# Kernel tuning notes

Measured on AMD Instinct MI355X. Metric: run time of the kernel, lower is better.

Reference implementation:

```python
import jax, jax.numpy as jnp
import numpy as np

NUM_HEADS = 12


def setup_inputs() -> dict:
    key = jax.random.key(0)
    ks = jax.random.split(key, 6)
    C = 768
    hd = C // NUM_HEADS  # 64
    H = W = 32
    x = jax.random.normal(ks[0], (4, H, W, C), dtype=jnp.float32)
    # Linear weights stored as (in, out) so y = x @ W (+ b)
    Wqkv = jax.random.normal(ks[1], (C, 3 * C), dtype=jnp.float32) * 0.02
    Wproj = jax.random.normal(ks[2], (C, C), dtype=jnp.float32) * 0.02
    bproj = jax.random.normal(ks[3], (C,), dtype=jnp.float32) * 0.02
    rel_pos_h = jax.random.normal(ks[4], (2 * H - 1, hd), dtype=jnp.float32) * 0.02
    rel_pos_w = jax.random.normal(ks[5], (2 * W - 1, hd), dtype=jnp.float32) * 0.02
    return {"x": x, "Wqkv": Wqkv, "Wproj": Wproj, "bproj": bproj,
            "rel_pos_h": rel_pos_h, "rel_pos_w": rel_pos_w}


def _get_rel_pos(size: int, rel_pos: jnp.ndarray) -> jnp.ndarray:
    # q_size == k_size == size; table already has 2*size-1 entries -> no interpolation
    coords = jnp.arange(size)[:, None] - jnp.arange(size)[None, :] + (size - 1)
    return rel_pos[coords]  # (size, size, head_dim)


def reference(x, Wqkv, Wproj, bproj, rel_pos_h, rel_pos_w):
    B, H, W, C = x.shape
    hn = NUM_HEADS
    hd = C // hn
    scale = hd ** (-0.5)
    S = H * W

    qkv = x @ Wqkv                                   # (B,H,W,3C)
    qkv = qkv.reshape(B, S, 3, hn, hd)
    qkv = jnp.transpose(qkv, (2, 0, 3, 1, 4)).reshape(3, B * hn, S, hd)
    q, k, v = qkv[0], qkv[1], qkv[2]                 # each (B*hn, S, hd)

    # decomposed relative position bias
    Rh = _get_rel_pos(H, rel_pos_h)                  # (H,H,hd)
    Rw = _get_rel_pos(W, rel_pos_w)                  # (W,W,hd)
    r_q = q.reshape(B * hn, H, W, hd)
    rel_h = jnp.einsum('bhwc,hkc->bhwk', r_q, Rh)    # (B*hn,H,W,H)
    rel_w = jnp.einsum('bhwc,wkc->bhwk', r_q, Rw)    # (B*hn,H,W,W)
    bias = rel_h[..., :, None] + rel_w[..., None, :] # (B*hn,H,W,H,W)
    bias = bias.reshape(B * hn, S, S)

    scores = scale * jnp.einsum('bqc,bkc->bqk', q, k) + bias
    attn = jax.nn.softmax(scores, axis=-1)
    out = jnp.einsum('bqk,bkc->bqc', attn, v)        # (B*hn,S,hd)

    out = out.reshape(B, hn, H, W, hd)
    out = jnp.transpose(out, (0, 2, 3, 1, 4)).reshape(B, H, W, C)
    return out @ Wproj + bproj
```

## Files before the change

kernel.cpp:

```cpp
#include <hip/hip_runtime.h>
#include <stddef.h>

typedef __bf16 bf16x8 __attribute__((ext_vector_type(8)));
typedef __bf16 bf16x4 __attribute__((ext_vector_type(4)));
typedef _Float16 f16x4 __attribute__((ext_vector_type(4)));
typedef float  f32x4  __attribute__((ext_vector_type(4)));

#define MFMA16(a, b, c) __builtin_amdgcn_mfma_f32_16x16x32_bf16((a), (b), (c), 0, 0, 0)
#define MFMA16H(a, b, c) __builtin_amdgcn_mfma_f32_16x16x16f16((a), (b), (c), 0, 0, 0)

__device__ __forceinline__ void gload_lds16(const void* gsrc, void* ldst) {
    __builtin_amdgcn_global_load_lds(
        (__attribute__((address_space(1))) void*)gsrc,
        (__attribute__((address_space(3))) void*)ldst,
        16, 0, 0);
}

__global__ void prep_kernel(const float* __restrict__ x, __bf16* __restrict__ xbf,
                            const float* __restrict__ Wqkv, __bf16* __restrict__ WqkvT,
                            const float* __restrict__ Wproj, __bf16* __restrict__ WprojT) {
    __shared__ float tile[32][33];
    const int bx = blockIdx.x, tid = threadIdx.x;
    if (bx < 3072) {
        int i = bx * 256 + tid;
        float4 v = ((const float4*)x)[i];
        bf16x4 o = {(__bf16)v.x, (__bf16)v.y, (__bf16)v.z, (__bf16)v.w};
        ((bf16x4*)xbf)[i] = o;
        return;
    }
    const float* in; __bf16* out; int R, C, c0, r0;
    if (bx < 4800) { int bb = bx - 3072; in = Wqkv;  out = WqkvT;  R = 768; C = 2304;
                     c0 = (bb % 72) * 32; r0 = (bb / 72) * 32; }
    else           { int bb = bx - 4800; in = Wproj; out = WprojT; R = 768; C = 768;
                     c0 = (bb % 24) * 32; r0 = (bb / 24) * 32; }
    const int tx = tid & 31, ty = tid >> 5;
#pragma unroll
    for (int i = 0; i < 32; i += 8)
        tile[ty + i][tx] = in[(size_t)(r0 + ty + i) * C + c0 + tx];
    __syncthreads();
#pragma unroll
    for (int i = 0; i < 32; i += 8)
        out[(size_t)(c0 + ty + i) * R + r0 + tx] = (__bf16)tile[tx][ty + i];
}

template<int BM, int BN>
__device__ __forceinline__ void gemm_core_bk64(
    const __bf16* __restrict__ A, const __bf16* __restrict__ Bt, int K,
    int m0, int n0, __bf16* aT, __bf16* bT, f32x4 (&acc)[BM/32][BN/32]) {
    const int tid  = threadIdx.x;
    const int wid  = tid >> 6, lane = tid & 63;
    const int quad = lane >> 4, l16 = lane & 15;
    const int wm = (wid >> 1) * (BM / 2), wn = (wid & 1) * (BN / 2);
    const int r_in = lane >> 3;
    const int cswz = ((lane & 7) ^ r_in) * 8;
    const __bf16* gA = A  + (size_t)(m0 + wid * 8 + r_in) * K + cswz;
    const __bf16* gB = Bt + (size_t)(n0 + wid * 8 + r_in) * K + cswz;
    const int sA = (l16 & 7);
    for (int k0 = 0; k0 < K; k0 += 64) {
        __syncthreads();
#pragma unroll
        for (int j = 0; j < BM / 32; j++)
            gload_lds16(gA + (size_t)(j * 32) * K + k0, aT + (j * 32 + wid * 8) * 64);
#pragma unroll
        for (int j = 0; j < BN / 32; j++)
            gload_lds16(gB + (size_t)(j * 32) * K + k0, bT + (j * 32 + wid * 8) * 64);
        __syncthreads();
#pragma unroll
        for (int kh = 0; kh < 2; kh++) {
            bf16x8 af[BM / 32], bfr[BN / 32];
            const int slot = ((kh * 4 + quad) ^ sA) << 3;
#pragma unroll
            for (int t = 0; t < BM / 32; t++)
                af[t]  = *(const bf16x8*)(aT + (wm + t * 16 + l16) * 64 + slot);
#pragma unroll
            for (int t = 0; t < BN / 32; t++)
                bfr[t] = *(const bf16x8*)(bT + (wn + t * 16 + l16) * 64 + slot);
#pragma unroll
            for (int rt = 0; rt < BM / 32; rt++)
#pragma unroll
                for (int ct = 0; ct < BN / 32; ct++)
                    acc[rt][ct] = MFMA16(af[rt], bfr[ct], acc[rt][ct]);
        }
    }
}

__global__ __launch_bounds__(256, 3)
void gemm_qkv_kernel(const __bf16* __restrict__ A, const __bf16* __restrict__ Bt,
                     __bf16* __restrict__ qb, __bf16* __restrict__ kb,
                     _Float16* __restrict__ vtb) {
    __shared__ __bf16 aT[8192], bT[6144];
    f32x4 acc[4][3];
#pragma unroll
    for (int i = 0; i < 4; i++)
#pragma unroll
        for (int j = 0; j < 3; j++) { f32x4 z = {0.f, 0.f, 0.f, 0.f}; acc[i][j] = z; }
    const int m0 = blockIdx.x * 128, n0 = blockIdx.y * 96;
    gemm_core_bk64<128, 96>(A, Bt, 768, m0, n0, aT, bT, acc);
    const int tid = threadIdx.x, wid = tid >> 6, lane = tid & 63;
    const int quad = lane >> 4, l16 = lane & 15;
    const int wm = (wid >> 1) * 64, wn = (wid & 1) * 48;
    const float KSCALE = 0.18033688f;
#pragma unroll
    for (int rt = 0; rt < 4; rt++)
#pragma unroll
        for (int ct = 0; ct < 3; ct++) {
            const int ng = n0 + wn + ct * 16 + l16;
            const int which = ng / 768;
            const int rem = ng - which * 768;
            const int hh = rem >> 6, d = rem & 63;
#pragma unroll
            for (int r = 0; r < 4; r++) {
                const int mg = m0 + wm + rt * 16 + quad * 4 + r;
                const int b = mg >> 10, s = mg & 1023;
                const int bh = b * 12 + hh;
                if (which == 0)      qb[((size_t)bh * 1024 + s) * 64 + d] = (__bf16)acc[rt][ct][r];
                else if (which == 1) kb[((size_t)bh * 1024 + s) * 64 + d] = (__bf16)(acc[rt][ct][r] * KSCALE);
                else                 vtb[((size_t)bh * 64 + d) * 1024 + s] = (_Float16)acc[rt][ct][r];
            }
        }
}

__global__ __launch_bounds__(256, 3)
void gemm_proj_kernel(const __bf16* __restrict__ A, const __bf16* __restrict__ Bt,
                      const float* __restrict__ bias, float* __restrict__ out) {
    __shared__ __bf16 aT[4096], bT[6144];
    f32x4 acc[2][3];
#pragma unroll
    for (int i = 0; i < 2; i++)
#pragma unroll
        for (int j = 0; j < 3; j++) { f32x4 z = {0.f, 0.f, 0.f, 0.f}; acc[i][j] = z; }
    const int m0 = blockIdx.x * 64, n0 = blockIdx.y * 96;
    gemm_core_bk64<64, 96>(A, Bt, 768, m0, n0, aT, bT, acc);
    const int tid = threadIdx.x, wid = tid >> 6, lane = tid & 63;
    const int quad = lane >> 4, l16 = lane & 15;
    const int wm = (wid >> 1) * 32, wn = (wid & 1) * 48;
#pragma unroll
    for (int rt = 0; rt < 2; rt++)
#pragma unroll
        for (int ct = 0; ct < 3; ct++) {
            const int ng = n0 + wn + ct * 16 + l16;
            const float bb = bias[ng];
#pragma unroll
            for (int r = 0; r < 4; r++) {
                const int mg = m0 + wm + rt * 16 + quad * 4 + r;
                out[(size_t)mg * 768 + ng] = acc[rt][ct][r] + bb;
            }
        }
}

__global__ __launch_bounds__(256, 3)
void attn_kernel(const __bf16* __restrict__ q, const __bf16* __restrict__ kk,
                 const _Float16* __restrict__ vt, const float* __restrict__ rph,
                 const float* __restrict__ rpw, __bf16* __restrict__ aout) {
    __shared__ __bf16   kbuf2[2][4096];
    __shared__ _Float16 vbuf2[2][4096];
    __shared__ float    relh[64][33];
    const int tid = threadIdx.x, wid = tid >> 6, lane = tid & 63;
    const int quad = lane >> 4, l16 = lane & 15;
    const int bh = blockIdx.x, qt = blockIdx.y;
    const int b = bh / 12, hh = bh - b * 12;
    const int q0 = qt * 64;
    const int w0 = wid * 16;
    const int h = qt * 2 + (wid >> 1);
    const float LOG2E = 1.44269504f;

    const __bf16* qp = q + ((size_t)bh * 1024 + q0 + w0 + l16) * 64;
    bf16x8 aq0 = *(const bf16x8*)(qp + quad * 8);
    bf16x8 aq1 = *(const bf16x8*)(qp + 32 + quad * 8);

    float* Dw = ((float*)kbuf2) + wid * 1024;
#pragma unroll
    for (int ct = 0; ct < 4; ct++) {
        int j = ct * 16 + l16; if (j > 62) j = 62;
        const float* tb = rpw + (size_t)j * 64;
        float4 t0 = *(const float4*)(tb + quad * 8);
        float4 t1 = *(const float4*)(tb + quad * 8 + 4);
        float4 t2 = *(const float4*)(tb + 32 + quad * 8);
        float4 t3 = *(const float4*)(tb + 32 + quad * 8 + 4);
        bf16x8 b0 = {(__bf16)(t0.x*LOG2E), (__bf16)(t0.y*LOG2E), (__bf16)(t0.z*LOG2E), (__bf16)(t0.w*LOG2E),
                     (__bf16)(t1.x*LOG2E), (__bf16)(t1.y*LOG2E), (__bf16)(t1.z*LOG2E), (__bf16)(t1.w*LOG2E)};
        bf16x8 b1 = {(__bf16)(t2.x*LOG2E), (__bf16)(t2.y*LOG2E), (__bf16)(t2.z*LOG2E), (__bf16)(t2.w*LOG2E),
                     (__bf16)(t3.x*LOG2E), (__bf16)(t3.y*LOG2E), (__bf16)(t3.z*LOG2E), (__bf16)(t3.w*LOG2E)};
        f32x4 z = {0.f, 0.f, 0.f, 0.f};
        z = MFMA16(aq0, b0, z);
        z = MFMA16(aq1, b1, z);
#pragma unroll
        for (int i = 0; i < 4; i++)
            Dw[(quad * 4 + i) * 64 + ct * 16 + l16] = z[i];
    }
#pragma unroll
    for (int ct = 0; ct < 2; ct++) {
        const int tr = h - (ct * 16 + l16) + 31;
        const float* tb = rph + (size_t)tr * 64;
        float4 t0 = *(const float4*)(tb + quad * 8);
        float4 t1 = *(const float4*)(tb + quad * 8 + 4);
        float4 t2 = *(const float4*)(tb + 32 + quad * 8);
        float4 t3 = *(const float4*)(tb + 32 + quad * 8 + 4);
        bf16x8 b0 = {(__bf16)(t0.x*LOG2E), (__bf16)(t0.y*LOG2E), (__bf16)(t0.z*LOG2E), (__bf16)(t0.w*LOG2E),
                     (__bf16)(t1.x*LOG2E), (__bf16)(t1.y*LOG2E), (__bf16)(t1.z*LOG2E), (__bf16)(t1.w*LOG2E)};
        bf16x8 b1 = {(__bf16)(t2.x*LOG2E), (__bf16)(t2.y*LOG2E), (__bf16)(t2.z*LOG2E), (__bf16)(t2.w*LOG2E),
                     (__bf16)(t3.x*LOG2E), (__bf16)(t3.y*LOG2E), (__bf16)(t3.z*LOG2E), (__bf16)(t3.w*LOG2E)};
        f32x4 z = {0.f, 0.f, 0.f, 0.f};
        z = MFMA16(aq0, b0, z);
        z = MFMA16(aq1, b1, z);
#pragma unroll
        for (int i = 0; i < 4; i++)
            relh[w0 + quad * 4 + i][ct * 16 + l16] = z[i];
    }
    const int wq = (wid & 1) * 16 + l16;
    float bw[2][4];
#pragma unroll
    for (int hf = 0; hf < 2; hf++)
#pragma unroll
        for (int r = 0; r < 4; r++)
            bw[hf][r] = Dw[l16 * 64 + wq + 31 - hf * 16 - quad * 4 - r];
    __syncthreads();

    float l_run = 0.f;
    f32x4 o_acc[4];
#pragma unroll
    for (int t = 0; t < 4; t++) { f32x4 z = {0.f, 0.f, 0.f, 0.f}; o_acc[t] = z; }

    const __bf16*   kg0 = kk + (size_t)bh * 65536;
    const _Float16* vg0 = vt + (size_t)bh * 65536;
    const int cbase = wid * 2;
    const int srow = lane >> 3;
    const int scol = ((lane & 7) ^ srow) * 8;
    const int swz0 = ((quad ^ (l16 & 7)) << 3);
    const int swz1 = (((quad | 4) ^ (l16 & 7)) << 3);
    const int l7 = l16 & 7, qhi = quad >> 1, qlo = (quad & 1) * 4;

    auto stage = [&](int buf, int kt) {
        const __bf16*   kg = kg0 + kt * 4096;
        const _Float16* vg = vg0 + kt * 64;
        __bf16*   kb_ = &kbuf2[buf][0];
        _Float16* vb_ = &vbuf2[buf][0];
#pragma unroll
        for (int j = 0; j < 2; j++) {
            const int c = cbase + j;
            gload_lds16(kg + (c * 8 + srow) * 64 + scol, kb_ + c * 512);
            gload_lds16(vg + (size_t)(c * 8 + srow) * 1024 + scol, vb_ + c * 512);
        }
    };

    stage(0, 0);
    for (int kt = 0; kt < 16; kt++) {
        const int cur = kt & 1;
        __syncthreads();
        if (kt < 15) stage(1 - cur, kt + 1);
        const __bf16*   kbuf = &kbuf2[cur][0];
        const _Float16* vbuf = &vbuf2[cur][0];

        f32x4 sacc[4];
#pragma unroll
        for (int ct = 0; ct < 4; ct++) {
            const int key = ct * 16 + l16;
            bf16x8 bk0 = *(const bf16x8*)(kbuf + key * 64 + swz0);
            bf16x8 bk1 = *(const bf16x8*)(kbuf + key * 64 + swz1);
            f32x4 z = {0.f, 0.f, 0.f, 0.f};
            z = MFMA16(bk0, aq0, z);
            z = MFMA16(bk1, aq1, z);
            sacc[ct] = z;
        }

        const float bh0 = relh[w0 + l16][kt * 2];
        const float bh1 = relh[w0 + l16][kt * 2 + 1];
        f16x4 pf[4];
#pragma unroll
        for (int ct = 0; ct < 4; ct++) {
            const float bhc = (ct < 2) ? bh0 : bh1;
#pragma unroll
            for (int r = 0; r < 4; r++) {
                float sv = sacc[ct][r] + (bhc + bw[ct & 1][r]);
                float p = __builtin_amdgcn_exp2f(sv);
                l_run += p;
                pf[ct][r] = (_Float16)p;
            }
        }

#pragma unroll
        for (int dt = 0; dt < 4; dt++) {
            const int vrow = (dt * 16 + l16) * 64;
#pragma unroll
            for (int ct = 0; ct < 4; ct++) {
                const int slot = (ct * 2 + qhi) ^ l7;
                f16x4 vf = *(const f16x4*)(vbuf + vrow + slot * 8 + qlo);
                o_acc[dt] = MFMA16H(vf, pf[ct], o_acc[dt]);
            }
        }
    }

    l_run += __shfl_xor(l_run, 16);
    l_run += __shfl_xor(l_run, 32);
    const float inv = 1.f / l_run;
    const int srow_o = q0 + w0 + l16;
#pragma unroll
    for (int dt = 0; dt < 4; dt++) {
        bf16x4 ov = {(__bf16)(o_acc[dt][0] * inv), (__bf16)(o_acc[dt][1] * inv),
                     (__bf16)(o_acc[dt][2] * inv), (__bf16)(o_acc[dt][3] * inv)};
        *(bf16x4*)&aout[((size_t)b * 1024 + srow_o) * 768 + hh * 64 + dt * 16 + quad * 4] = ov;
    }
}

extern "C" void kernel_launch(void* const* d_in, const int* in_sizes, int n_in,
                              void* d_out, int out_size, void* d_ws, size_t ws_size,
                              hipStream_t stream) {
    const float* x     = (const float*)d_in[0];
    const float* Wqkv  = (const float*)d_in[1];
    const float* Wproj = (const float*)d_in[2];
    const float* bproj = (const float*)d_in[3];
    const float* rph   = (const float*)d_in[4];
    const float* rpw   = (const float*)d_in[5];
    float* out = (float*)d_out;
    char* ws = (char*)d_ws;

    __bf16*   xbf    = (__bf16*)(ws);
    __bf16*   WqkvT  = (__bf16*)(ws + 6291456);
    __bf16*   WprojT = (__bf16*)(ws + 9830400);
    __bf16*   qb     = (__bf16*)(ws + 11010048);
    __bf16*   kb     = (__bf16*)(ws + 17301504);
    _Float16* vtb    = (_Float16*)(ws + 23592960);
    __bf16*   aob    = (__bf16*)(ws + 29884416);

    prep_kernel<<<dim3(5376), dim3(256), 0, stream>>>(x, xbf, Wqkv, WqkvT, Wproj, WprojT);
    gemm_qkv_kernel<<<dim3(32, 24), dim3(256), 0, stream>>>(xbf, WqkvT, qb, kb, vtb);
    attn_kernel<<<dim3(48, 16), dim3(256), 0, stream>>>(qb, kb, vtb, rph, rpw, aob);
    gemm_proj_kernel<<<dim3(64, 8), dim3(256), 0, stream>>>(aob, WprojT, bproj, out);
}
```

Baseline: 142.0 us.

## Double-buffer GEMM LDS tiles with BK=32 to overlap loads and MFMA

```diff
diff --git a/kernel.cpp b/kernel.cpp
--- a/kernel.cpp
+++ b/kernel.cpp
@@ -44,43 +44,52 @@
 }
 
 template<int BM, int BN>
-__device__ __forceinline__ void gemm_core_bk64(
+__device__ __forceinline__ void gemm_core_bk32(
     const __bf16* __restrict__ A, const __bf16* __restrict__ Bt, int K,
     int m0, int n0, __bf16* aT, __bf16* bT, f32x4 (&acc)[BM/32][BN/32]) {
     const int tid  = threadIdx.x;
     const int wid  = tid >> 6, lane = tid & 63;
     const int quad = lane >> 4, l16 = lane & 15;
     const int wm = (wid >> 1) * (BM / 2), wn = (wid & 1) * (BN / 2);
-    const int r_in = lane >> 3;
-    const int cswz = ((lane & 7) ^ r_in) * 8;
-    const __bf16* gA = A  + (size_t)(m0 + wid * 8 + r_in) * K + cswz;
-    const __bf16* gB = Bt + (size_t)(n0 + wid * 8 + r_in) * K + cswz;
-    const int sA = (l16 & 7);
-    for (int k0 = 0; k0 < K; k0 += 64) {
+    const int srow = tid >> 2;
+    const int schunk = ((tid & 3) ^ (srow & 3)) * 8;
+    const __bf16* gA = A  + (size_t)(m0 + srow) * K + schunk;
+    const __bf16* gB = Bt + (size_t)(n0 + srow) * K + schunk;
+    const int fslot = (quad ^ (l16 & 3)) * 8;
+    const int ABUF = BM * 32, BBUF = BN * 32;
+
+    auto stage = [&](int buf, int k0) {
+        __bf16* aD = aT + buf * ABUF;
+        __bf16* bD = bT + buf * BBUF;
+#pragma unroll
+        for (int j = 0; j < BM / 64; j++)
+            gload_lds16(gA + (size_t)(j * 64) * K + k0, aD + (j * 64 + wid * 16) * 32);
+        gload_lds16(gB + k0, bD + wid * 16 * 32);
+        if (tid < 128)
+            gload_lds16(gB + (size_t)64 * K + k0, bD + (64 + wid * 16) * 32);
+    };
+
+    stage(0, 0);
+    const int NK = K / 32;
+#pragma unroll 2
+    for (int k = 0; k < NK; k++) {
+        const int cur = k & 1;
         __syncthreads();
-#pragma unroll
-        for (int j = 0; j < BM / 32; j++)
-            gload_lds16(gA + (size_t)(j * 32) * K + k0, aT + (j * 32 + wid * 8) * 64);
-#pragma unroll
-        for (int j = 0; j < BN / 32; j++)
-            gload_lds16(gB + (size_t)(j * 32) * K + k0, bT + (j * 32 + wid * 8) * 64);
-        __syncthreads();
-#pragma unroll
-        for (int kh = 0; kh < 2; kh++) {
-            bf16x8 af[BM / 32], bfr[BN / 32];
-            const int slot = ((kh * 4 + quad) ^ sA) << 3;
-#pragma unroll
-            for (int t = 0; t < BM / 32; t++)
-                af[t]  = *(const bf16x8*)(aT + (wm + t * 16 + l16) * 64 + slot);
-#pragma unroll
-            for (int t = 0; t < BN / 32; t++)
-                bfr[t] = *(const bf16x8*)(bT + (wn + t * 16 + l16) * 64 + slot);
-#pragma unroll
-            for (int rt = 0; rt < BM / 32; rt++)
-#pragma unroll
-                for (int ct = 0; ct < BN / 32; ct++)
-                    acc[rt][ct] = MFMA16(af[rt], bfr[ct], acc[rt][ct]);
-        }
+        if (k < NK - 1) stage(cur ^ 1, (k + 1) * 32);
+        const __bf16* aS = aT + cur * ABUF;
+        const __bf16* bS = bT + cur * BBUF;
+        bf16x8 af[BM / 32], bfr[BN / 32];
+#pragma unroll
+        for (int t = 0; t < BM / 32; t++)
+            af[t]  = *(const bf16x8*)(aS + (wm + t * 16 + l16) * 32 + fslot);
+#pragma unroll
+        for (int t = 0; t < BN / 32; t++)
+            bfr[t] = *(const bf16x8*)(bS + (wn + t * 16 + l16) * 32 + fslot);
+#pragma unroll
+        for (int rt = 0; rt < BM / 32; rt++)
+#pragma unroll
+            for (int ct = 0; ct < BN / 32; ct++)
+                acc[rt][ct] = MFMA16(af[rt], bfr[ct], acc[rt][ct]);
     }
 }
 
@@ -88,14 +97,14 @@
 void gemm_qkv_kernel(const __bf16* __restrict__ A, const __bf16* __restrict__ Bt,
                      __bf16* __restrict__ qb, __bf16* __restrict__ kb,
                      _Float16* __restrict__ vtb) {
-    __shared__ __bf16 aT[8192], bT[6144];
+    __shared__ __bf16 aT[2 * 128 * 32], bT[2 * 96 * 32];
     f32x4 acc[4][3];
 #pragma unroll
     for (int i = 0; i < 4; i++)
 #pragma unroll
         for (int j = 0; j < 3; j++) { f32x4 z = {0.f, 0.f, 0.f, 0.f}; acc[i][j] = z; }
     const int m0 = blockIdx.x * 128, n0 = blockIdx.y * 96;
-    gemm_core_bk64<128, 96>(A, Bt, 768, m0, n0, aT, bT, acc);
+    gemm_core_bk32<128, 96>(A, Bt, 768, m0, n0, aT, bT, acc);
     const int tid = threadIdx.x, wid = tid >> 6, lane = tid & 63;
     const int quad = lane >> 4, l16 = lane & 15;
     const int wm = (wid >> 1) * 64, wn = (wid & 1) * 48;
@@ -123,14 +132,14 @@
 __global__ __launch_bounds__(256, 3)
 void gemm_proj_kernel(const __bf16* __restrict__ A, const __bf16* __restrict__ Bt,
                       const float* __restrict__ bias, float* __restrict__ out) {
-    __shared__ __bf16 aT[4096], bT[6144];
+    __shared__ __bf16 aT[2 * 64 * 32], bT[2 * 96 * 32];
     f32x4 acc[2][3];
 #pragma unroll
     for (int i = 0; i < 2; i++)
 #pragma unroll
         for (int j = 0; j < 3; j++) { f32x4 z = {0.f, 0.f, 0.f, 0.f}; acc[i][j] = z; }
     const int m0 = blockIdx.x * 64, n0 = blockIdx.y * 96;
-    gemm_core_bk64<64, 96>(A, Bt, 768, m0, n0, aT, bT, acc);
+    gemm_core_bk32<64, 96>(A, Bt, 768, m0, n0, aT, bT, acc);
     const int tid = threadIdx.x, wid = tid >> 6, lane = tid & 63;
     const int quad = lane >> 4, l16 = lane & 15;
     const int wm = (wid >> 1) * 32, wn = (wid & 1) * 48;
```

Measured after the change: 149.2 us. 1.05x slower.
